# Optimization experiments

Hardware: AMD Instinct MI355X
Metric: run time of the kernel (lower is better)

The kernel has to match this reference:

```python
import jax, jax.numpy as jnp
import numpy as np

BLOCK = 64      # base classifier input height/width
STRIDE = 16     # BLOCK // 4 per Windowing(stride=[1,bh/4,bw/4,1], size=[1,bh,bw,1])
K = 10          # n_classes
THRESH = 0.7    # bbox_threshold


def extract_patches(x):
    # x: [B,H,W,C] -> [B,R,Cc,BLOCK*BLOCK*C], same layout as tf.image.extract_patches
    B, H, Wd, C = x.shape
    R = (H - BLOCK) // STRIDE + 1
    Cc = (Wd - BLOCK) // STRIDE + 1
    rows = jnp.arange(R)[:, None] * STRIDE + jnp.arange(BLOCK)[None, :]   # [R,64]
    cols = jnp.arange(Cc)[:, None] * STRIDE + jnp.arange(BLOCK)[None, :]  # [Cc,64]
    p = x[:, rows]                 # [B,R,64,W,C]
    p = p[:, :, :, cols]           # [B,R,64,Cc,64,C]
    p = jnp.transpose(p, (0, 1, 3, 2, 4, 5))  # [B,R,Cc,64,64,C]
    return p.reshape(B, R, Cc, BLOCK * BLOCK * C)


def connected_components(mask):
    # 4-connected components of a 2D bool mask via iterative min-label propagation.
    # Background = 0; foreground labels are distinct positive ints per component.
    R, C = mask.shape
    big = jnp.int32(R * C + 2)
    init = jnp.where(mask, jnp.arange(1, R * C + 1, dtype=jnp.int32).reshape(R, C), 0)

    def step(lab, _):
        l = jnp.where(mask, lab, big)
        up = jnp.concatenate([jnp.full((1, C), big, l.dtype), l[:-1]], 0)
        dn = jnp.concatenate([l[1:], jnp.full((1, C), big, l.dtype)], 0)
        lf = jnp.concatenate([jnp.full((R, 1), big, l.dtype), l[:, :-1]], 1)
        rt = jnp.concatenate([l[:, 1:], jnp.full((R, 1), big, l.dtype)], 1)
        m = jnp.minimum(jnp.minimum(l, jnp.minimum(up, dn)), jnp.minimum(lf, rt))
        return jnp.where(mask, m, 0), None

    lab, _ = jax.lax.scan(step, init, None, length=2 * (R + C))
    return lab


def boxes_from_labels(lab):
    # Segmented min/max over label ids replaces the per-region python loop:
    # box = [rowmin-1, colmin-1, rowmax+1, colmax+1] per component.
    R, C = lab.shape
    N = R * C
    flat = lab.reshape(N)
    rr = jnp.arange(N, dtype=jnp.int32) // C
    cc = jnp.arange(N, dtype=jnp.int32) % C
    rmin = jax.ops.segment_min(rr, flat, num_segments=N + 1)
    cmin = jax.ops.segment_min(cc, flat, num_segments=N + 1)
    rmax = jax.ops.segment_max(rr, flat, num_segments=N + 1)
    cmax = jax.ops.segment_max(cc, flat, num_segments=N + 1)
    cnt = jax.ops.segment_sum(jnp.ones(N, jnp.int32), flat, num_segments=N + 1)
    valid = (cnt > 0).at[0].set(False)  # slot 0 is background
    boxes = jnp.stack([rmin - 1, cmin - 1, rmax + 1, cmax + 1], -1)
    boxes = jnp.where(valid[:, None], boxes, 0)
    return boxes, valid


def setup_inputs() -> dict:
    key = jax.random.key(0)
    k1, k2, k3 = jax.random.split(key, 3)
    inputs = jax.random.normal(k1, (1, 1024, 1024, 3), dtype=jnp.float32)
    # scale W so logits have ~unit variance -> sparse (realistic) threshold mask
    W = jax.random.normal(k2, (12288, K), dtype=jnp.float32) * 0.01
    b = jax.random.normal(k3, (K,), dtype=jnp.float32)
    return {"inputs": inputs, "W": W, "b": b}


def reference(inputs, W, b):
    patches = extract_patches(inputs)               # [1,R,Cc,D]
    B, R, Cc, D = patches.shape
    logits = patches.reshape(B * R * Cc, D) @ W + b # [N,K]
    prob = jax.nn.softmax(logits, axis=1).reshape(R, Cc, K)
    mask = prob > THRESH                            # [R,Cc,K]
    labels = jax.vmap(connected_components, in_axes=2, out_axes=2)(mask)  # [R,Cc,K]
    boxes, valid = jax.vmap(boxes_from_labels)(jnp.transpose(labels, (2, 0, 1)))
    # boxes: [K, R*Cc+1, 4] padded per-component bboxes; valid: [K, R*Cc+1]
    return prob, labels, boxes, valid
```

## Files before the change

### kernel.cpp

```cpp
#include <hip/hip_runtime.h>
#include <cmath>

#define RR 61
#define NCELL 3721
#define KCLS 10
#define DDIM 12288
#define BIGV 0x0FFFFFFF
#define PITCH 64

#define OUT_PROB 0
#define OUT_LAB  37210
#define OUT_BOX  74420
#define OUT_VALID 223300

__global__ __launch_bounds__(1024) void k1_logits(
    const float* __restrict__ x, const float* __restrict__ W,
    const float* __restrict__ b, float* __restrict__ out)
{
    const int tid  = threadIdx.x;
    const int tsub = tid & 255;
    const int wrow = tid >> 8;
    const int blk  = blockIdx.x;
    const int rg   = blk >> 4;
    const int cg   = blk & 15;

    int r = rg * 4 + wrow; if (r > 60) r = 60;
    const int c0 = cg * 4;

    float acc[4][KCLS];
#pragma unroll
    for (int p = 0; p < 4; ++p)
#pragma unroll
        for (int k = 0; k < KCLS; ++k) acc[p][k] = 0.0f;

    int coff[4];
#pragma unroll
    for (int p = 0; p < 4; ++p) {
        int c = c0 + p; if (c > 60) c = 60;
        coff[p] = c * 48;
    }
    const int rbase = r * 49152;

    int i   = (tsub >= 192) ? 1 : 0;
    int rem = tsub - i * 192;

#pragma unroll 2
    for (int it = 0; it < 48; ++it) {
        const int d = tsub + (it << 8);
        const float* xp = x + rbase + i * 3072 + rem;
        float xv[4];
#pragma unroll
        for (int p = 0; p < 4; ++p) xv[p] = xp[coff[p]];

        const float2* wp = (const float2*)(W + (size_t)d * KCLS);
        const float2 w0 = wp[0], w1 = wp[1], w2 = wp[2], w3 = wp[3], w4 = wp[4];
        const float wv[KCLS] = { w0.x, w0.y, w1.x, w1.y, w2.x, w2.y,
                                 w3.x, w3.y, w4.x, w4.y };
#pragma unroll
        for (int p = 0; p < 4; ++p)
#pragma unroll
            for (int k = 0; k < KCLS; ++k) acc[p][k] += xv[p] * wv[k];

        rem += 64; ++i;
        if (rem >= 192) { rem -= 192; ++i; }
    }

#pragma unroll
    for (int p = 0; p < 4; ++p)
#pragma unroll
        for (int k = 0; k < KCLS; ++k) {
            float v = acc[p][k];
#pragma unroll
            for (int off = 32; off > 0; off >>= 1) v += __shfl_down(v, off);
            acc[p][k] = v;
        }

    __shared__ float red[4][4][4][KCLS];
    const int wgrp = (tsub >> 6);
    if ((tsub & 63) == 0) {
#pragma unroll
        for (int p = 0; p < 4; ++p)
#pragma unroll
            for (int k = 0; k < KCLS; ++k) red[wrow][wgrp][p][k] = acc[p][k];
    }
    __syncthreads();

    if (tid < 16) {
        const int wr = tid >> 2;
        const int p  = tid & 3;
        const int rr = rg * 4 + wr;
        const int cc = c0 + p;
        if (rr <= 60 && cc <= 60) {
            double l[KCLS];
#pragma unroll
            for (int k = 0; k < KCLS; ++k)
                l[k] = (double)red[wr][0][p][k] + (double)red[wr][1][p][k]
                     + (double)red[wr][2][p][k] + (double)red[wr][3][p][k]
                     + (double)b[k];
            double m = l[0];
#pragma unroll
            for (int k = 1; k < KCLS; ++k) m = fmax(m, l[k]);
            double e[KCLS], s = 0.0;
#pragma unroll
            for (int k = 0; k < KCLS; ++k) { e[k] = exp(l[k] - m); s += e[k]; }
            const double inv = 1.0 / s;
            float* po = out + OUT_PROB + (size_t)(rr * 61 + cc) * KCLS;
#pragma unroll
            for (int k = 0; k < KCLS; ++k) po[k] = (float)(e[k] * inv);
        }
    }
}

__global__ __launch_bounds__(1024) void k2_cc_boxes(float* __restrict__ out)
{
    const int k   = blockIdx.x;
    const int tid = threadIdx.x;

    __shared__ int lab[63 * PITCH];
    __shared__ int act[NCELL];
    __shared__ int nact;
    __shared__ int changed;
    __shared__ int rmn[NCELL + 1], rmx[NCELL + 1], cmn[NCELL + 1], cmx[NCELL + 1];

    for (int idx = tid; idx < 63 * PITCH; idx += 1024) lab[idx] = BIGV;
    for (int s = tid; s <= NCELL; s += 1024) {
        rmn[s] = 0x7fffffff; cmn[s] = 0x7fffffff; rmx[s] = -1; cmx[s] = -1;
    }
    if (tid == 0) nact = 0;
    __syncthreads();

    for (int idx = tid; idx < NCELL; idx += 1024) {
        const float pv = out[OUT_PROB + (size_t)idx * KCLS + k];
        if (pv > 0.7f) {
            const int r = idx / 61, c = idx - r * 61;
            const int off = (r + 1) * PITCH + (c + 1);
            lab[off] = idx + 1;
            act[atomicAdd(&nact, 1)] = off;
        }
    }
    __syncthreads();
    const int na = nact;

    for (int iter = 0; iter < 600; ++iter) {
        if (tid == 0) changed = 0;
        __syncthreads();
        bool ch = false;
        for (int idx = tid; idx < na; idx += 1024) {
            const int off = act[idx];
            int v = lab[off];
            int t;
            t = lab[off - 1];     if (t < v) v = t;
            t = lab[off + 1];     if (t < v) v = t;
            t = lab[off - PITCH]; if (t < v) v = t;
            t = lab[off + PITCH]; if (t < v) v = t;
            if (v < lab[off]) { lab[off] = v; ch = true; }
        }
        if (ch) changed = 1;
        __syncthreads();
        if (changed == 0) break;
        __syncthreads();
    }

    for (int idx = tid; idx < na; idx += 1024) {
        const int off = act[idx];
        const int lb  = lab[off];
        const int r = (off >> 6) - 1, c = (off & 63) - 1;
        atomicMin(&rmn[lb], r); atomicMax(&rmx[lb], r);
        atomicMin(&cmn[lb], c); atomicMax(&cmx[lb], c);
    }
    __syncthreads();

    for (int idx = tid; idx < NCELL; idx += 1024) {
        const int r = idx / 61, c = idx - r * 61;
        const int v = lab[(r + 1) * PITCH + (c + 1)];
        out[OUT_LAB + (size_t)idx * KCLS + k] = (float)((v < BIGV) ? v : 0);
    }
    for (int s = tid; s <= NCELL; s += 1024) {
        const bool val = (s > 0) && (rmx[s] >= 0);
        float* bo = out + OUT_BOX + (size_t)(k * (NCELL + 1) + s) * 4;
        if (val) {
            bo[0] = (float)(rmn[s] - 1);
            bo[1] = (float)(cmn[s] - 1);
            bo[2] = (float)(rmx[s] + 1);
            bo[3] = (float)(cmx[s] + 1);
        } else {
            bo[0] = 0.0f; bo[1] = 0.0f; bo[2] = 0.0f; bo[3] = 0.0f;
        }
        out[OUT_VALID + (size_t)k * (NCELL + 1) + s] = val ? 1.0f : 0.0f;
    }
}

extern "C" void kernel_launch(void* const* d_in, const int* in_sizes, int n_in,
                              void* d_out, int out_size, void* d_ws, size_t ws_size,
                              hipStream_t stream) {
    const float* x = (const float*)d_in[0];
    const float* W = (const float*)d_in[1];
    const float* b = (const float*)d_in[2];
    float* out = (float*)d_out;

    k1_logits  <<<dim3(256), dim3(1024), 0, stream>>>(x, W, b, out);
    k2_cc_boxes<<<dim3(KCLS), dim3(1024), 0, stream>>>(out);
}
```

Before: 105.1 us.

## Stage W in LDS per chunk and replace label propagation with union-find

The logits kernel now copies W into shared memory in six transposed, padded chunks and reads weights from LDS rather than from global memory on every iteration. This cuts repeated global/L2 weight traffic at the cost of extra barriers and staging work. The connected-components kernel replaces the iterative min-label propagation loop, which synchronises every iteration, with a lock-free union-find in shared memory. Labels are the min root index plus one, which matches the reference min-label semantics.

Result: slower. 108.0 us (+2.7%).

```diff
diff --git a/kernel.cpp b/kernel.cpp
--- a/kernel.cpp
+++ b/kernel.cpp
@@ -5,13 +5,13 @@
 #define NCELL 3721
 #define KCLS 10
 #define DDIM 12288
-#define BIGV 0x0FFFFFFF
-#define PITCH 64
 
 #define OUT_PROB 0
 #define OUT_LAB  37210
 #define OUT_BOX  74420
 #define OUT_VALID 223300
+
+#define WPAD 2052
 
 __global__ __launch_bounds__(1024) void k1_logits(
     const float* __restrict__ x, const float* __restrict__ W,
@@ -24,6 +24,9 @@
     const int rg   = blk >> 4;
     const int cg   = blk & 15;
 
+    __shared__ float wlds[KCLS * WPAD];
+    __shared__ float red[4][4][4][KCLS];
+
     int r = rg * 4 + wrow; if (r > 60) r = 60;
     const int c0 = cg * 4;
 
@@ -44,25 +47,34 @@
     int i   = (tsub >= 192) ? 1 : 0;
     int rem = tsub - i * 192;
 
-#pragma unroll 2
-    for (int it = 0; it < 48; ++it) {
-        const int d = tsub + (it << 8);
-        const float* xp = x + rbase + i * 3072 + rem;
-        float xv[4];
-#pragma unroll
-        for (int p = 0; p < 4; ++p) xv[p] = xp[coff[p]];
-
-        const float2* wp = (const float2*)(W + (size_t)d * KCLS);
-        const float2 w0 = wp[0], w1 = wp[1], w2 = wp[2], w3 = wp[3], w4 = wp[4];
-        const float wv[KCLS] = { w0.x, w0.y, w1.x, w1.y, w2.x, w2.y,
-                                 w3.x, w3.y, w4.x, w4.y };
-#pragma unroll
-        for (int p = 0; p < 4; ++p)
-#pragma unroll
-            for (int k = 0; k < KCLS; ++k) acc[p][k] += xv[p] * wv[k];
-
-        rem += 64; ++i;
-        if (rem >= 192) { rem -= 192; ++i; }
+    for (int chunk = 0; chunk < 6; ++chunk) {
+        __syncthreads();
+        for (int f = tid; f < 20480; f += 1024) {
+            const int ff = chunk * 20480 + f;
+            const int d  = ff / 10;
+            const int kk = ff - d * 10;
+            wlds[kk * WPAD + (d - (chunk << 11))] = W[ff];
+        }
+        __syncthreads();
+
+#pragma unroll
+        for (int it = 0; it < 8; ++it) {
+            const int dl = tsub + (it << 8);
+            const float* xp = x + rbase + i * 3072 + rem;
+            float xv[4];
+#pragma unroll
+            for (int p = 0; p < 4; ++p) xv[p] = xp[coff[p]];
+            float wv[KCLS];
+#pragma unroll
+            for (int k = 0; k < KCLS; ++k) wv[k] = wlds[k * WPAD + dl];
+#pragma unroll
+            for (int p = 0; p < 4; ++p)
+#pragma unroll
+                for (int k = 0; k < KCLS; ++k) acc[p][k] += xv[p] * wv[k];
+
+            rem += 64; ++i;
+            if (rem >= 192) { rem -= 192; ++i; }
+        }
     }
 
 #pragma unroll
@@ -75,7 +87,6 @@
             acc[p][k] = v;
         }
 
-    __shared__ float red[4][4][4][KCLS];
     const int wgrp = (tsub >> 6);
     if ((tsub & 63) == 0) {
 #pragma unroll
@@ -111,70 +122,70 @@
     }
 }
 
+__device__ __forceinline__ int uf_find(int* par, int xx) {
+    int x = xx;
+    while (true) {
+        const int p = ((volatile int*)par)[x];
+        if (p == x) return x;
+        const int gp = ((volatile int*)par)[p];
+        if (gp == p) return p;
+        atomicCAS(&par[x], p, gp);
+        x = gp;
+    }
+}
+
+__device__ __forceinline__ void uf_union(int* par, int a, int b) {
+    int ra = uf_find(par, a);
+    int rb = uf_find(par, b);
+    while (ra != rb) {
+        if (ra < rb) { const int t = ra; ra = rb; rb = t; }
+        const int old = atomicMin(&par[ra], rb);
+        if (old == ra || old == rb) break;
+        const int hi = old > rb ? old : rb;
+        const int lo = old ^ rb ^ hi;
+        ra = uf_find(par, hi);
+        rb = uf_find(par, lo);
+    }
+}
+
 __global__ __launch_bounds__(1024) void k2_cc_boxes(float* __restrict__ out)
 {
     const int k   = blockIdx.x;
     const int tid = threadIdx.x;
 
-    __shared__ int lab[63 * PITCH];
-    __shared__ int act[NCELL];
-    __shared__ int nact;
-    __shared__ int changed;
+    __shared__ int par[NCELL];
     __shared__ int rmn[NCELL + 1], rmx[NCELL + 1], cmn[NCELL + 1], cmx[NCELL + 1];
 
-    for (int idx = tid; idx < 63 * PITCH; idx += 1024) lab[idx] = BIGV;
     for (int s = tid; s <= NCELL; s += 1024) {
         rmn[s] = 0x7fffffff; cmn[s] = 0x7fffffff; rmx[s] = -1; cmx[s] = -1;
     }
-    if (tid == 0) nact = 0;
-    __syncthreads();
-
     for (int idx = tid; idx < NCELL; idx += 1024) {
         const float pv = out[OUT_PROB + (size_t)idx * KCLS + k];
-        if (pv > 0.7f) {
+        par[idx] = (pv > 0.7f) ? idx : -1;
+    }
+    __syncthreads();
+
+    for (int idx = tid; idx < NCELL; idx += 1024) {
+        if (par[idx] < 0) continue;
+        const int r = idx / 61, c = idx - r * 61;
+        if (c > 0  && par[idx - 1]  >= 0) uf_union(par, idx, idx - 1);
+        if (r > 0  && par[idx - 61] >= 0) uf_union(par, idx, idx - 61);
+    }
+    __syncthreads();
+
+    for (int idx = tid; idx < NCELL; idx += 1024) {
+        int lab = 0;
+        if (par[idx] >= 0) {
+            const int root = uf_find(par, idx);
+            lab = root + 1;
             const int r = idx / 61, c = idx - r * 61;
-            const int off = (r + 1) * PITCH + (c + 1);
-            lab[off] = idx + 1;
-            act[atomicAdd(&nact, 1)] = off;
-        }
-    }
-    __syncthreads();
-    const int na = nact;
-
-    for (int iter = 0; iter < 600; ++iter) {
-        if (tid == 0) changed = 0;
-        __syncthreads();
-        bool ch = false;
-        for (int idx = tid; idx < na; idx += 1024) {
-            const int off = act[idx];
-            int v = lab[off];
-            int t;
-            t = lab[off - 1];     if (t < v) v = t;
-            t = lab[off + 1];     if (t < v) v = t;
-            t = lab[off - PITCH]; if (t < v) v = t;
-            t = lab[off + PITCH]; if (t < v) v = t;
-            if (v < lab[off]) { lab[off] = v; ch = true; }
-        }
-        if (ch) changed = 1;
-        __syncthreads();
-        if (changed == 0) break;
-        __syncthreads();
-    }
-
-    for (int idx = tid; idx < na; idx += 1024) {
-        const int off = act[idx];
-        const int lb  = lab[off];
-        const int r = (off >> 6) - 1, c = (off & 63) - 1;
-        atomicMin(&rmn[lb], r); atomicMax(&rmx[lb], r);
-        atomicMin(&cmn[lb], c); atomicMax(&cmx[lb], c);
-    }
-    __syncthreads();
-
-    for (int idx = tid; idx < NCELL; idx += 1024) {
-        const int r = idx / 61, c = idx - r * 61;
-        const int v = lab[(r + 1) * PITCH + (c + 1)];
-        out[OUT_LAB + (size_t)idx * KCLS + k] = (float)((v < BIGV) ? v : 0);
-    }
+            atomicMin(&rmn[lab], r); atomicMax(&rmx[lab], r);
+            atomicMin(&cmn[lab], c); atomicMax(&cmx[lab], c);
+        }
+        out[OUT_LAB + (size_t)idx * KCLS + k] = (float)lab;
+    }
+    __syncthreads();
+
     for (int s = tid; s <= NCELL; s += 1024) {
         const bool val = (s > 0) && (rmx[s] >= 0);
         float* bo = out + OUT_BOX + (size_t)(k * (NCELL + 1) + s) * 4;
```
